# Optimization experiments

Measured on AMD Instinct MI355X. Metric: run time of the kernel, lower is better.

Reference implementation:

```python
import jax, jax.numpy as jnp
import numpy as np

# Gate hyperparameters (from init_kwargs)
DIM = 4096
N_EXPERTS = 256        # n_routed_experts
N_GROUPS = 8           # n_expert_groups
TOPK_GROUPS = 4        # n_limited_groups
TOPK = 8               # n_activated_experts
ROUTE_SCALE = 1.0
N_TOKENS = 16384       # batch * seq_len flattened


def setup_inputs() -> dict:
    key = jax.random.key(0)
    kx, kw = jax.random.split(key)
    x = jax.random.normal(kx, (N_TOKENS, DIM), dtype=jnp.float32)
    # xavier-ish scale for the gate projection weight [n_experts, dim]
    weight = jax.random.normal(kw, (N_EXPERTS, DIM), dtype=jnp.float32) * (1.0 / np.sqrt(DIM))
    return {"x": x, "weight": weight}


def reference(x, weight):
    T = x.shape[0]
    # scores = linear(x, weight)  -> [T, E]
    logits = jnp.einsum('td,ed->te', x, weight)
    # score_func == 'softmax' computed in fp32 (torch: softmax(dim=-1, dtype=float32))
    scores = jax.nn.softmax(logits.astype(jnp.float32), axis=-1)
    original_scores = scores

    # group-limited routing (n_groups > 1, no bias -> amax per group)
    sg = scores.reshape(T, N_GROUPS, N_EXPERTS // N_GROUPS)   # [T, G, E/G]
    group_scores = jnp.max(sg, axis=-1)                        # [T, G]
    _, gidx = jax.lax.top_k(group_scores, TOPK_GROUPS)         # [T, topk_groups]
    keep = jnp.zeros((T, N_GROUPS), dtype=bool)
    keep = keep.at[jnp.arange(T)[:, None], gidx].set(True)
    masked = jnp.where(keep[:, :, None], sg, -jnp.inf).reshape(T, N_EXPERTS)

    # top-k expert selection; weights gathered from the un-masked scores
    _, idx = jax.lax.top_k(masked, TOPK)                       # [T, topk]
    weights = jnp.take_along_axis(original_scores, idx, axis=1)
    weights = weights * ROUTE_SCALE
    return weights.astype(x.dtype), idx
```

## Files before the change

### kernel.cpp

```cpp
#include <hip/hip_runtime.h>
#include <math.h>
#include <stdint.h>

#define NTOK   16384
#define DIM    4096
#define NEXP   256
#define TOPKG  4
#define TOPK   8
#define NSPLIT 4
#define KCHUNK (DIM / NSPLIT)
#define BM     256
#define BK     32
#define NSTEPS (KCHUNK / BK)

typedef float v4f   __attribute__((ext_vector_type(4)));
typedef short short8 __attribute__((ext_vector_type(8)));

__device__ inline unsigned short f2bf(float x) {
    unsigned u = __float_as_uint(x);
    return (unsigned short)((u + 0x7fffu + ((u >> 16) & 1u)) >> 16);
}
__device__ inline float bf2f(unsigned short h) {
    return __uint_as_float(((unsigned)h) << 16);
}

__global__ __launch_bounds__(256) void wprep(const float* __restrict__ W,
                                             unsigned short* __restrict__ Wh,
                                             unsigned short* __restrict__ Wl) {
    int i = (blockIdx.x * 256 + threadIdx.x) * 4;
    float4 v = *(const float4*)(W + i);
    ushort4 h, l;
    h.x = f2bf(v.x); l.x = f2bf(v.x - bf2f(h.x));
    h.y = f2bf(v.y); l.y = f2bf(v.y - bf2f(h.y));
    h.z = f2bf(v.z); l.z = f2bf(v.z - bf2f(h.z));
    h.w = f2bf(v.w); l.w = f2bf(v.w - bf2f(h.w));
    *(ushort4*)(Wh + i) = h;
    *(ushort4*)(Wl + i) = l;
}

__global__ __launch_bounds__(512, 2) void gate_gemm(const float* __restrict__ X,
                                                    const unsigned short* __restrict__ Wh,
                                                    const unsigned short* __restrict__ Wl,
                                                    float* __restrict__ P) {
    __shared__ __align__(16) unsigned short Ah[2][BM * BK];
    __shared__ __align__(16) unsigned short Al[2][BM * BK];
    __shared__ __align__(16) unsigned short Bh[2][NEXP * BK];
    __shared__ __align__(16) unsigned short Bl[2][NEXP * BK];

    const int t  = threadIdx.x;
    const int bm = blockIdx.x * BM;
    const int z  = blockIdx.y;
    const int k0 = z * KCHUNK;

    const int l  = t & 63;
    const int w  = t >> 6;
    const int wr = w >> 2;
    const int wc = w & 3;
    const int lm = l & 15;
    const int lq = l >> 4;

    const int ar = t >> 1;
    const int ak = (t & 1) * 16;
    const float* xrow = X + (size_t)(bm + ar) * DIM + k0 + ak;

    v4f acc[8][4] = {};

    {
#pragma unroll
        for (int i = 0; i < 2; ++i) {
            int flat = i * 512 + t;
            int e = flat >> 2, q = flat & 3;
            const unsigned short* gh = Wh + (size_t)e * DIM + k0 + q * 8;
            const unsigned short* gl = Wl + (size_t)e * DIM + k0 + q * 8;
            __builtin_amdgcn_global_load_lds(
                (const __attribute__((address_space(1))) unsigned int*)gh,
                (__attribute__((address_space(3))) unsigned int*)&Bh[0][flat * 8], 16, 0, 0);
            __builtin_amdgcn_global_load_lds(
                (const __attribute__((address_space(1))) unsigned int*)gl,
                (__attribute__((address_space(3))) unsigned int*)&Bl[0][flat * 8], 16, 0, 0);
        }
        float4 xv[4];
#pragma unroll
        for (int i = 0; i < 4; ++i) xv[i] = *(const float4*)(xrow + i * 4);
#pragma unroll
        for (int i = 0; i < 4; ++i) {
            ushort4 h, lo;
            h.x = f2bf(xv[i].x); lo.x = f2bf(xv[i].x - bf2f(h.x));
            h.y = f2bf(xv[i].y); lo.y = f2bf(xv[i].y - bf2f(h.y));
            h.z = f2bf(xv[i].z); lo.z = f2bf(xv[i].z - bf2f(h.z));
            h.w = f2bf(xv[i].w); lo.w = f2bf(xv[i].w - bf2f(h.w));
            *(ushort4*)&Ah[0][ar * BK + ak + i * 4] = h;
            *(ushort4*)&Al[0][ar * BK + ak + i * 4] = lo;
        }
        __syncthreads();
    }

    int p = 0;
    for (int s = 0; s < NSTEPS; ++s) {
        const int krn = (s + 1 < NSTEPS ? s + 1 : s) * BK;

        float4 xv[4];
#pragma unroll
        for (int i = 0; i < 4; ++i) xv[i] = *(const float4*)(xrow + krn + i * 4);
#pragma unroll
        for (int i = 0; i < 2; ++i) {
            int flat = i * 512 + t;
            int e = flat >> 2, q = flat & 3;
            const unsigned short* gh = Wh + (size_t)e * DIM + k0 + krn + q * 8;
            const unsigned short* gl = Wl + (size_t)e * DIM + k0 + krn + q * 8;
            __builtin_amdgcn_global_load_lds(
                (const __attribute__((address_space(1))) unsigned int*)gh,
                (__attribute__((address_space(3))) unsigned int*)&Bh[p ^ 1][flat * 8], 16, 0, 0);
            __builtin_amdgcn_global_load_lds(
                (const __attribute__((address_space(1))) unsigned int*)gl,
                (__attribute__((address_space(3))) unsigned int*)&Bl[p ^ 1][flat * 8], 16, 0, 0);
        }

        short8 bh[4], bl[4];
#pragma unroll
        for (int c = 0; c < 4; ++c) {
            int e = wc * 64 + c * 16 + lm;
            bh[c] = *(const short8*)&Bh[p][e * BK + lq * 8];
            bl[c] = *(const short8*)&Bl[p][e * BK + lq * 8];
        }
#pragma unroll
        for (int r = 0; r < 8; ++r) {
            int m = wr * 128 + r * 16 + lm;
            short8 ah = *(const short8*)&Ah[p][m * BK + lq * 8];
            short8 al = *(const short8*)&Al[p][m * BK + lq * 8];
#pragma unroll
            for (int c = 0; c < 4; ++c) {
                acc[r][c] = __builtin_amdgcn_mfma_f32_16x16x32_bf16(ah, bh[c], acc[r][c], 0, 0, 0);
                acc[r][c] = __builtin_amdgcn_mfma_f32_16x16x32_bf16(ah, bl[c], acc[r][c], 0, 0, 0);
                acc[r][c] = __builtin_amdgcn_mfma_f32_16x16x32_bf16(al, bh[c], acc[r][c], 0, 0, 0);
            }
        }

        __builtin_amdgcn_sched_barrier(0);

#pragma unroll
        for (int i = 0; i < 4; ++i) {
            ushort4 h, lo;
            h.x = f2bf(xv[i].x); lo.x = f2bf(xv[i].x - bf2f(h.x));
            h.y = f2bf(xv[i].y); lo.y = f2bf(xv[i].y - bf2f(h.y));
            h.z = f2bf(xv[i].z); lo.z = f2bf(xv[i].z - bf2f(h.z));
            h.w = f2bf(xv[i].w); lo.w = f2bf(xv[i].w - bf2f(h.w));
            *(ushort4*)&Ah[p ^ 1][ar * BK + ak + i * 4] = h;
            *(ushort4*)&Al[p ^ 1][ar * BK + ak + i * 4] = lo;
        }

        __syncthreads();
        p ^= 1;
    }

    float* Pb = P + ((size_t)z * NTOK + bm) * NEXP;
#pragma unroll
    for (int r = 0; r < 8; ++r)
#pragma unroll
        for (int c = 0; c < 4; ++c)
#pragma unroll
            for (int g = 0; g < 4; ++g)
                Pb[(size_t)(wr * 128 + r * 16 + lq * 4 + g) * NEXP + wc * 64 + c * 16 + lm] = acc[r][c][g];
}

__global__ __launch_bounds__(256) void gate_route(const float* __restrict__ P,
                                                  float* __restrict__ outw,
                                                  float* __restrict__ outi) {
    const int lane = threadIdx.x & 63;
    const int tok  = (blockIdx.x * blockDim.x + threadIdx.x) >> 6;
    if (tok >= NTOK) return;

    float l[4] = {0.f, 0.f, 0.f, 0.f};
#pragma unroll
    for (int z = 0; z < NSPLIT; ++z) {
        float4 v = *(const float4*)(P + ((size_t)z * NTOK + tok) * NEXP + lane * 4);
        l[0] += v.x; l[1] += v.y; l[2] += v.z; l[3] += v.w;
    }

    float lmax = fmaxf(fmaxf(l[0], l[1]), fmaxf(l[2], l[3]));
    float m = lmax;
#pragma unroll
    for (int o = 32; o; o >>= 1) m = fmaxf(m, __shfl_xor(m, o));

    float s = __expf(l[0] - m) + __expf(l[1] - m) + __expf(l[2] - m) + __expf(l[3] - m);
#pragma unroll
    for (int o = 32; o; o >>= 1) s += __shfl_xor(s, o);

    float gm = lmax;
#pragma unroll
    for (int o = 4; o; o >>= 1) gm = fmaxf(gm, __shfl_xor(gm, o));

    const int g = lane >> 3;
    int rank = 0;
#pragma unroll
    for (int gg = 0; gg < 8; ++gg) {
        float vg = __shfl(gm, gg * 8);
        rank += (vg > gm) || (vg == gm && gg < g);
    }
    const bool allowed = rank < TOPKG;

    float mv[4];
#pragma unroll
    for (int j = 0; j < 4; ++j) mv[j] = allowed ? l[j] : -INFINITY;

    float wsel = 0.0f;
    int   isel = 0;

    for (int k = 0; k < TOPK; ++k) {
        float bv = mv[0];
        int   bi = lane * 4;
        if (mv[1] > bv) { bv = mv[1]; bi = lane * 4 + 1; }
        if (mv[2] > bv) { bv = mv[2]; bi = lane * 4 + 2; }
        if (mv[3] > bv) { bv = mv[3]; bi = lane * 4 + 3; }
#pragma unroll
        for (int o = 32; o; o >>= 1) {
            float ov = __shfl_xor(bv, o);
            int   oi = __shfl_xor(bi, o);
            if (ov > bv || (ov == bv && oi < bi)) { bv = ov; bi = oi; }
        }
        if (lane == k) { wsel = __expf(bv - m) / s; isel = bi; }
        if ((bi >> 2) == lane) mv[bi & 3] = -INFINITY;
    }

    if (lane < TOPK) {
        outw[(size_t)tok * TOPK + lane] = wsel;
        outi[(size_t)tok * TOPK + lane] = (float)isel;
    }
}

extern "C" void kernel_launch(void* const* d_in, const int* in_sizes, int n_in,
                              void* d_out, int out_size, void* d_ws, size_t ws_size,
                              hipStream_t stream) {
    const float* x  = (const float*)d_in[0];
    const float* wt = (const float*)d_in[1];

    float* P = (float*)d_ws;
    unsigned short* Wh = (unsigned short*)((char*)d_ws + (size_t)NSPLIT * NTOK * NEXP * 4);
    unsigned short* Wl = Wh + (size_t)NEXP * DIM;

    float* outw = (float*)d_out;
    float* outi = (float*)d_out + (size_t)NTOK * TOPK;

    wprep<<<(NEXP * DIM) / (256 * 4), 256, 0, stream>>>(wt, Wh, Wl);

    dim3 ggrid(NTOK / BM, NSPLIT);
    gate_gemm<<<ggrid, 512, 0, stream>>>(x, Wh, Wl, P);

    gate_route<<<(NTOK * 64) / 256, 256, 0, stream>>>(P, outw, outi);
}
```

Before: 444.3 us.

## Swizzle LDS tiles and interleave prefetch with MFMA in four barrier-separated phases

Applies an XOR swizzle to the LDS layout of the A and B hi/lo tiles, applied consistently to global source offsets and LDS reads, to reduce bank conflicts on short8 reads. Splits each K-step into four phases, each doing two row-tiles of MFMAs. The global_load_lds for Wh and Wl, the X loads and the bf16 split conversions are spread across those phases, with s_barrier, lgkmcnt waits and setprio around the MFMA clusters. This aims to overlap memory and conversion work with matrix math, at the cost of more barriers per step and fragile waitcnt reasoning.

```diff
diff --git a/kernel.cpp b/kernel.cpp
--- a/kernel.cpp
+++ b/kernel.cpp
@@ -23,6 +23,7 @@
 __device__ inline float bf2f(unsigned short h) {
     return __uint_as_float(((unsigned)h) << 16);
 }
+__device__ inline int swz4(int row, int slot) { return slot ^ ((row >> 1) & 3); }
 
 __global__ __launch_bounds__(256) void wprep(const float* __restrict__ W,
                                              unsigned short* __restrict__ Wh,
@@ -60,8 +61,7 @@
     const int lq = l >> 4;
 
     const int ar = t >> 1;
-    const int ak = (t & 1) * 16;
-    const float* xrow = X + (size_t)(bm + ar) * DIM + k0 + ak;
+    const float* xrow = X + (size_t)(bm + ar) * DIM + k0 + (t & 1) * 16;
 
     v4f acc[8][4] = {};
 
@@ -69,9 +69,9 @@
 #pragma unroll
         for (int i = 0; i < 2; ++i) {
             int flat = i * 512 + t;
-            int e = flat >> 2, q = flat & 3;
-            const unsigned short* gh = Wh + (size_t)e * DIM + k0 + q * 8;
-            const unsigned short* gl = Wl + (size_t)e * DIM + k0 + q * 8;
+            int e = flat >> 2, qq = flat & 3;
+            const unsigned short* gh = Wh + (size_t)e * DIM + k0 + swz4(e, qq) * 8;
+            const unsigned short* gl = Wl + (size_t)e * DIM + k0 + swz4(e, qq) * 8;
             __builtin_amdgcn_global_load_lds(
                 (const __attribute__((address_space(1))) unsigned int*)gh,
                 (__attribute__((address_space(3))) unsigned int*)&Bh[0][flat * 8], 16, 0, 0);
@@ -79,78 +79,112 @@
                 (const __attribute__((address_space(1))) unsigned int*)gl,
                 (__attribute__((address_space(3))) unsigned int*)&Bl[0][flat * 8], 16, 0, 0);
         }
-        float4 xv[4];
-#pragma unroll
-        for (int i = 0; i < 4; ++i) xv[i] = *(const float4*)(xrow + i * 4);
+        float4 xv0[4];
+#pragma unroll
+        for (int i = 0; i < 4; ++i) xv0[i] = *(const float4*)(xrow + i * 4);
 #pragma unroll
         for (int i = 0; i < 4; ++i) {
             ushort4 h, lo;
-            h.x = f2bf(xv[i].x); lo.x = f2bf(xv[i].x - bf2f(h.x));
-            h.y = f2bf(xv[i].y); lo.y = f2bf(xv[i].y - bf2f(h.y));
-            h.z = f2bf(xv[i].z); lo.z = f2bf(xv[i].z - bf2f(h.z));
-            h.w = f2bf(xv[i].w); lo.w = f2bf(xv[i].w - bf2f(h.w));
-            *(ushort4*)&Ah[0][ar * BK + ak + i * 4] = h;
-            *(ushort4*)&Al[0][ar * BK + ak + i * 4] = lo;
+            h.x = f2bf(xv0[i].x); lo.x = f2bf(xv0[i].x - bf2f(h.x));
+            h.y = f2bf(xv0[i].y); lo.y = f2bf(xv0[i].y - bf2f(h.y));
+            h.z = f2bf(xv0[i].z); lo.z = f2bf(xv0[i].z - bf2f(h.z));
+            h.w = f2bf(xv0[i].w); lo.w = f2bf(xv0[i].w - bf2f(h.w));
+            int j = (t & 1) * 4 + i;
+            int idx = ar * BK + swz4(ar, j >> 1) * 8 + (j & 1) * 4;
+            *(ushort4*)&Ah[0][idx] = h;
+            *(ushort4*)&Al[0][idx] = lo;
         }
         __syncthreads();
     }
 
-    int p = 0;
+    int cur = 0;
     for (int s = 0; s < NSTEPS; ++s) {
-        const int krn = (s + 1 < NSTEPS ? s + 1 : s) * BK;
-
+        const int nxt = cur ^ 1;
+        const bool pf = (s + 1 < NSTEPS);
+        const int krn = (pf ? s + 1 : s) * BK;
+
+        short8 bh[4], bl[4];
         float4 xv[4];
-#pragma unroll
-        for (int i = 0; i < 4; ++i) xv[i] = *(const float4*)(xrow + krn + i * 4);
-#pragma unroll
-        for (int i = 0; i < 2; ++i) {
-            int flat = i * 512 + t;
-            int e = flat >> 2, q = flat & 3;
-            const unsigned short* gh = Wh + (size_t)e * DIM + k0 + krn + q * 8;
-            const unsigned short* gl = Wl + (size_t)e * DIM + k0 + krn + q * 8;
-            __builtin_amdgcn_global_load_lds(
-                (const __attribute__((address_space(1))) unsigned int*)gh,
-                (__attribute__((address_space(3))) unsigned int*)&Bh[p ^ 1][flat * 8], 16, 0, 0);
-            __builtin_amdgcn_global_load_lds(
-                (const __attribute__((address_space(1))) unsigned int*)gl,
-                (__attribute__((address_space(3))) unsigned int*)&Bl[p ^ 1][flat * 8], 16, 0, 0);
-        }
-
-        short8 bh[4], bl[4];
-#pragma unroll
-        for (int c = 0; c < 4; ++c) {
-            int e = wc * 64 + c * 16 + lm;
-            bh[c] = *(const short8*)&Bh[p][e * BK + lq * 8];
-            bl[c] = *(const short8*)&Bl[p][e * BK + lq * 8];
-        }
-#pragma unroll
-        for (int r = 0; r < 8; ++r) {
-            int m = wr * 128 + r * 16 + lm;
-            short8 ah = *(const short8*)&Ah[p][m * BK + lq * 8];
-            short8 al = *(const short8*)&Al[p][m * BK + lq * 8];
+
+#pragma unroll
+        for (int q = 0; q < 4; ++q) {
+            if (q == 0) {
+#pragma unroll
+                for (int c = 0; c < 4; ++c) {
+                    int e = wc * 64 + c * 16 + lm;
+                    bh[c] = *(const short8*)&Bh[cur][e * BK + swz4(e, lq) * 8];
+                    bl[c] = *(const short8*)&Bl[cur][e * BK + swz4(e, lq) * 8];
+                }
+            }
+            const int m0 = wr * 128 + (2 * q) * 16 + lm;
+            const int m1 = m0 + 16;
+            short8 a0h = *(const short8*)&Ah[cur][m0 * BK + swz4(m0, lq) * 8];
+            short8 a0l = *(const short8*)&Al[cur][m0 * BK + swz4(m0, lq) * 8];
+            short8 a1h = *(const short8*)&Ah[cur][m1 * BK + swz4(m1, lq) * 8];
+            short8 a1l = *(const short8*)&Al[cur][m1 * BK + swz4(m1, lq) * 8];
+
+            if (pf) {
+                if (q == 0) {
+#pragma unroll
+                    for (int i = 0; i < 4; ++i) xv[i] = *(const float4*)(xrow + krn + i * 4);
+#pragma unroll
+                    for (int i = 0; i < 2; ++i) {
+                        int flat = i * 512 + t;
+                        int e = flat >> 2, qq = flat & 3;
+                        const unsigned short* g = Wh + (size_t)e * DIM + k0 + krn + swz4(e, qq) * 8;
+                        __builtin_amdgcn_global_load_lds(
+                            (const __attribute__((address_space(1))) unsigned int*)g,
+                            (__attribute__((address_space(3))) unsigned int*)&Bh[nxt][flat * 8], 16, 0, 0);
+                    }
+                } else if (q == 1) {
+#pragma unroll
+                    for (int i = 0; i < 2; ++i) {
+                        int flat = i * 512 + t;
+                        int e = flat >> 2, qq = flat & 3;
+                        const unsigned short* g = Wl + (size_t)e * DIM + k0 + krn + swz4(e, qq) * 8;
+                        __builtin_amdgcn_global_load_lds(
+                            (const __attribute__((address_space(1))) unsigned int*)g,
+                            (__attribute__((address_space(3))) unsigned int*)&Bl[nxt][flat * 8], 16, 0, 0);
+                    }
+                } else {
+                    const int i0 = (q == 2) ? 0 : 2;
+#pragma unroll
+                    for (int i = i0; i < i0 + 2; ++i) {
+                        ushort4 h, lo;
+                        h.x = f2bf(xv[i].x); lo.x = f2bf(xv[i].x - bf2f(h.x));
+                        h.y = f2bf(xv[i].y); lo.y = f2bf(xv[i].y - bf2f(h.y));
+                        h.z = f2bf(xv[i].z); lo.z = f2bf(xv[i].z - bf2f(h.z));
+                        h.w = f2bf(xv[i].w); lo.w = f2bf(xv[i].w - bf2f(h.w));
+                        int j = (t & 1) * 4 + i;
+                        int idx = ar * BK + swz4(ar, j >> 1) * 8 + (j & 1) * 4;
+                        *(ushort4*)&Ah[nxt][idx] = h;
+                        *(ushort4*)&Al[nxt][idx] = lo;
+                    }
+                }
+            }
+
+            if (q == 0) asm volatile("s_waitcnt lgkmcnt(8)");
+            __builtin_amdgcn_s_barrier();
+            asm volatile("s_waitcnt lgkmcnt(0)");
+            __builtin_amdgcn_sched_barrier(0);
+            __builtin_amdgcn_s_setprio(1);
 #pragma unroll
             for (int c = 0; c < 4; ++c) {
-                acc[r][c] = __builtin_amdgcn_mfma_f32_16x16x32_bf16(ah, bh[c], acc[r][c], 0, 0, 0);
-                acc[r][c] = __builtin_amdgcn_mfma_f32_16x16x32_bf16(ah, bl[c], acc[r][c], 0, 0, 0);
-                acc[r][c] = __builtin_amdgcn_mfma_f32_16x16x32_bf16(al, bh[c], acc[r][c], 0, 0, 0);
-            }
-        }
-
-        __builtin_amdgcn_sched_barrier(0);
-
-#pragma unroll
-        for (int i = 0; i < 4; ++i) {
-            ushort4 h, lo;
-            h.x = f2bf(xv[i].x); lo.x = f2bf(xv[i].x - bf2f(h.x));
-            h.y = f2bf(xv[i].y); lo.y = f2bf(xv[i].y - bf2f(h.y));
-            h.z = f2bf(xv[i].z); lo.z = f2bf(xv[i].z - bf2f(h.z));
-            h.w = f2bf(xv[i].w); lo.w = f2bf(xv[i].w - bf2f(h.w));
-            *(ushort4*)&Ah[p ^ 1][ar * BK + ak + i * 4] = h;
-            *(ushort4*)&Al[p ^ 1][ar * BK + ak + i * 4] = lo;
-        }
-
-        __syncthreads();
-        p ^= 1;
+                acc[2 * q][c] = __builtin_amdgcn_mfma_f32_16x16x32_bf16(a0h, bh[c], acc[2 * q][c], 0, 0, 0);
+                acc[2 * q][c] = __builtin_amdgcn_mfma_f32_16x16x32_bf16(a0h, bl[c], acc[2 * q][c], 0, 0, 0);
+                acc[2 * q][c] = __builtin_amdgcn_mfma_f32_16x16x32_bf16(a0l, bh[c], acc[2 * q][c], 0, 0, 0);
+            }
+#pragma unroll
+            for (int c = 0; c < 4; ++c) {
+                acc[2 * q + 1][c] = __builtin_amdgcn_mfma_f32_16x16x32_bf16(a1h, bh[c], acc[2 * q + 1][c], 0, 0, 0);
+                acc[2 * q + 1][c] = __builtin_amdgcn_mfma_f32_16x16x32_bf16(a1h, bl[c], acc[2 * q + 1][c], 0, 0, 0);
+                acc[2 * q + 1][c] = __builtin_amdgcn_mfma_f32_16x16x32_bf16(a1l, bh[c], acc[2 * q + 1][c], 0, 0, 0);
+            }
+            __builtin_amdgcn_s_setprio(0);
+            if (q < 3) __builtin_amdgcn_s_barrier();
+            else       __syncthreads();
+        }
+        cur = nxt;
     }
 
     float* Pb = P + ((size_t)z * NTOK + bm) * NEXP;
```

New measurement: 438.6 us. About the same (-1.3%).

## Load X fragments straight to registers, shrink M tile, swizzle W LDS layout

Applied to the files above, without the earlier changes.

Drops the LDS staging of the X tile. Each wave now loads its own fp32 X rows straight into registers and splits them into bf16 hi/lo MFMA operands there. The M tile shrinks from 256 to 128 rows and launch bounds rise to 4 blocks per CU to raise occupancy. The W tiles get an XOR swizzle to cut LDS bank conflicts, and the MFMA section runs at raised wave priority. In exchange, X is read from global with no overlap from a prior prefetch, each W tile is reused across fewer rows, and W global traffic doubles because the grid has twice as many blocks.

```diff
diff --git a/kernel.cpp b/kernel.cpp
--- a/kernel.cpp
+++ b/kernel.cpp
@@ -9,7 +9,7 @@
 #define TOPK   8
 #define NSPLIT 4
 #define KCHUNK (DIM / NSPLIT)
-#define BM     256
+#define BM     128
 #define BK     32
 #define NSTEPS (KCHUNK / BK)
 
@@ -23,6 +23,7 @@
 __device__ inline float bf2f(unsigned short h) {
     return __uint_as_float(((unsigned)h) << 16);
 }
+__device__ inline int swz4(int row, int slot) { return slot ^ ((row >> 1) & 3); }
 
 __global__ __launch_bounds__(256) void wprep(const float* __restrict__ W,
                                              unsigned short* __restrict__ Wh,
@@ -38,12 +39,10 @@
     *(ushort4*)(Wl + i) = l;
 }
 
-__global__ __launch_bounds__(512, 2) void gate_gemm(const float* __restrict__ X,
+__global__ __launch_bounds__(512, 4) void gate_gemm(const float* __restrict__ X,
                                                     const unsigned short* __restrict__ Wh,
                                                     const unsigned short* __restrict__ Wl,
                                                     float* __restrict__ P) {
-    __shared__ __align__(16) unsigned short Ah[2][BM * BK];
-    __shared__ __align__(16) unsigned short Al[2][BM * BK];
     __shared__ __align__(16) unsigned short Bh[2][NEXP * BK];
     __shared__ __align__(16) unsigned short Bl[2][NEXP * BK];
 
@@ -59,108 +58,99 @@
     const int lm = l & 15;
     const int lq = l >> 4;
 
-    const int ar = t >> 1;
-    const int ak = (t & 1) * 16;
-    const float* xrow = X + (size_t)(bm + ar) * DIM + k0 + ak;
-
-    v4f acc[8][4] = {};
-
-    {
-#pragma unroll
-        for (int i = 0; i < 2; ++i) {
-            int flat = i * 512 + t;
-            int e = flat >> 2, q = flat & 3;
-            const unsigned short* gh = Wh + (size_t)e * DIM + k0 + q * 8;
-            const unsigned short* gl = Wl + (size_t)e * DIM + k0 + q * 8;
-            __builtin_amdgcn_global_load_lds(
-                (const __attribute__((address_space(1))) unsigned int*)gh,
-                (__attribute__((address_space(3))) unsigned int*)&Bh[0][flat * 8], 16, 0, 0);
-            __builtin_amdgcn_global_load_lds(
-                (const __attribute__((address_space(1))) unsigned int*)gl,
-                (__attribute__((address_space(3))) unsigned int*)&Bl[0][flat * 8], 16, 0, 0);
-        }
-        float4 xv[4];
-#pragma unroll
-        for (int i = 0; i < 4; ++i) xv[i] = *(const float4*)(xrow + i * 4);
-#pragma unroll
-        for (int i = 0; i < 4; ++i) {
-            ushort4 h, lo;
-            h.x = f2bf(xv[i].x); lo.x = f2bf(xv[i].x - bf2f(h.x));
-            h.y = f2bf(xv[i].y); lo.y = f2bf(xv[i].y - bf2f(h.y));
-            h.z = f2bf(xv[i].z); lo.z = f2bf(xv[i].z - bf2f(h.z));
-            h.w = f2bf(xv[i].w); lo.w = f2bf(xv[i].w - bf2f(h.w));
-            *(ushort4*)&Ah[0][ar * BK + ak + i * 4] = h;
-            *(ushort4*)&Al[0][ar * BK + ak + i * 4] = lo;
-        }
-        __syncthreads();
-    }
-
-    int p = 0;
+    const float* xbase = X + (size_t)(bm + wr * 64 + lm) * DIM + k0 + lq * 8;
+
+    v4f acc[4][4] = {};
+
+#pragma unroll
+    for (int i = 0; i < 2; ++i) {
+        int flat = i * 512 + t;
+        int e = flat >> 2, qq = flat & 3;
+        const unsigned short* gh = Wh + (size_t)e * DIM + k0 + swz4(e, qq) * 8;
+        const unsigned short* gl = Wl + (size_t)e * DIM + k0 + swz4(e, qq) * 8;
+        __builtin_amdgcn_global_load_lds(
+            (const __attribute__((address_space(1))) unsigned int*)gh,
+            (__attribute__((address_space(3))) unsigned int*)&Bh[0][flat * 8], 16, 0, 0);
+        __builtin_amdgcn_global_load_lds(
+            (const __attribute__((address_space(1))) unsigned int*)gl,
+            (__attribute__((address_space(3))) unsigned int*)&Bl[0][flat * 8], 16, 0, 0);
+    }
+    __syncthreads();
+
+    int cur = 0;
     for (int s = 0; s < NSTEPS; ++s) {
-        const int krn = (s + 1 < NSTEPS ? s + 1 : s) * BK;
-
-        float4 xv[4];
-#pragma unroll
-        for (int i = 0; i < 4; ++i) xv[i] = *(const float4*)(xrow + krn + i * 4);
-#pragma unroll
-        for (int i = 0; i < 2; ++i) {
-            int flat = i * 512 + t;
-            int e = flat >> 2, q = flat & 3;
-            const unsigned short* gh = Wh + (size_t)e * DIM + k0 + krn + q * 8;
-            const unsigned short* gl = Wl + (size_t)e * DIM + k0 + krn + q * 8;
-            __builtin_amdgcn_global_load_lds(
-                (const __attribute__((address_space(1))) unsigned int*)gh,
-                (__attribute__((address_space(3))) unsigned int*)&Bh[p ^ 1][flat * 8], 16, 0, 0);
-            __builtin_amdgcn_global_load_lds(
-                (const __attribute__((address_space(1))) unsigned int*)gl,
-                (__attribute__((address_space(3))) unsigned int*)&Bl[p ^ 1][flat * 8], 16, 0, 0);
-        }
+        const int nxt = cur ^ 1;
+        const bool pf = (s + 1 < NSTEPS);
+
+        float4 a0[4], a1[4];
+#pragma unroll
+        for (int r = 0; r < 4; ++r) {
+            const float* p = xbase + (size_t)r * 16 * DIM + s * BK;
+            a0[r] = *(const float4*)p;
+            a1[r] = *(const float4*)(p + 4);
+        }
+
+        if (pf) {
+            const int krn = (s + 1) * BK;
+#pragma unroll
+            for (int i = 0; i < 2; ++i) {
+                int flat = i * 512 + t;
+                int e = flat >> 2, qq = flat & 3;
+                const unsigned short* gh = Wh + (size_t)e * DIM + k0 + krn + swz4(e, qq) * 8;
+                const unsigned short* gl = Wl + (size_t)e * DIM + k0 + krn + swz4(e, qq) * 8;
+                __builtin_amdgcn_global_load_lds(
+                    (const __attribute__((address_space(1))) unsigned int*)gh,
+                    (__attribute__((address_space(3))) unsigned int*)&Bh[nxt][flat * 8], 16, 0, 0);
+                __builtin_amdgcn_global_load_lds(
+                    (const __attribute__((address_space(1))) unsigned int*)gl,
+                    (__attribute__((address_space(3))) unsigned int*)&Bl[nxt][flat * 8], 16, 0, 0);
+            }
+        }
+        __builtin_amdgcn_sched_barrier(0);
 
         short8 bh[4], bl[4];
 #pragma unroll
         for (int c = 0; c < 4; ++c) {
             int e = wc * 64 + c * 16 + lm;
-            bh[c] = *(const short8*)&Bh[p][e * BK + lq * 8];
-            bl[c] = *(const short8*)&Bl[p][e * BK + lq * 8];
-        }
-#pragma unroll
-        for (int r = 0; r < 8; ++r) {
-            int m = wr * 128 + r * 16 + lm;
-            short8 ah = *(const short8*)&Ah[p][m * BK + lq * 8];
-            short8 al = *(const short8*)&Al[p][m * BK + lq * 8];
+            bh[c] = *(const short8*)&Bh[cur][e * BK + swz4(e, lq) * 8];
+            bl[c] = *(const short8*)&Bl[cur][e * BK + swz4(e, lq) * 8];
+        }
+
+        short8 ah[4], al[4];
+#pragma unroll
+        for (int r = 0; r < 4; ++r) {
+#pragma unroll
+            for (int j = 0; j < 8; ++j) {
+                float x = (j < 4) ? ((const float*)&a0[r])[j] : ((const float*)&a1[r])[j - 4];
+                unsigned short h = f2bf(x);
+                ah[r][j] = (short)h;
+                al[r][j] = (short)f2bf(x - bf2f(h));
+            }
+        }
+
+        __builtin_amdgcn_s_setprio(1);
+#pragma unroll
+        for (int r = 0; r < 4; ++r)
 #pragma unroll
             for (int c = 0; c < 4; ++c) {
-                acc[r][c] = __builtin_amdgcn_mfma_f32_16x16x32_bf16(ah, bh[c], acc[r][c], 0, 0, 0);
-                acc[r][c] = __builtin_amdgcn_mfma_f32_16x16x32_bf16(ah, bl[c], acc[r][c], 0, 0, 0);
-                acc[r][c] = __builtin_amdgcn_mfma_f32_16x16x32_bf16(al, bh[c], acc[r][c], 0, 0, 0);
+                acc[r][c] = __builtin_amdgcn_mfma_f32_16x16x32_bf16(ah[r], bh[c], acc[r][c], 0, 0, 0);
+                acc[r][c] = __builtin_amdgcn_mfma_f32_16x16x32_bf16(ah[r], bl[c], acc[r][c], 0, 0, 0);
+                acc[r][c] = __builtin_amdgcn_mfma_f32_16x16x32_bf16(al[r], bh[c], acc[r][c], 0, 0, 0);
             }
-        }
-
-        __builtin_amdgcn_sched_barrier(0);
-
-#pragma unroll
-        for (int i = 0; i < 4; ++i) {
-            ushort4 h, lo;
-            h.x = f2bf(xv[i].x); lo.x = f2bf(xv[i].x - bf2f(h.x));
-            h.y = f2bf(xv[i].y); lo.y = f2bf(xv[i].y - bf2f(h.y));
-            h.z = f2bf(xv[i].z); lo.z = f2bf(xv[i].z - bf2f(h.z));
-            h.w = f2bf(xv[i].w); lo.w = f2bf(xv[i].w - bf2f(h.w));
-            *(ushort4*)&Ah[p ^ 1][ar * BK + ak + i * 4] = h;
-            *(ushort4*)&Al[p ^ 1][ar * BK + ak + i * 4] = lo;
-        }
+        __builtin_amdgcn_s_setprio(0);
 
         __syncthreads();
-        p ^= 1;
+        cur = nxt;
     }
 
     float* Pb = P + ((size_t)z * NTOK + bm) * NEXP;
 #pragma unroll
-    for (int r = 0; r < 8; ++r)
+    for (int r = 0; r < 4; ++r)
 #pragma unroll
         for (int c = 0; c < 4; ++c)
 #pragma unroll
             for (int g = 0; g < 4; ++g)
-                Pb[(size_t)(wr * 128 + r * 16 + lq * 4 + g) * NEXP + wc * 64 + c * 16 + lm] = acc[r][c][g];
+                Pb[(size_t)(wr * 64 + r * 16 + lq * 4 + g) * NEXP + wc * 64 + c * 16 + lm] = acc[r][c][g];
 }
 
 __global__ __launch_bounds__(256) void gate_route(const float* __restrict__ P,
```

Result: slower. 1.170 ms (+163.3%).
